# Kernel optimization log

Measured on AMD Instinct MI355X. Metric: run time of the kernel, lower is better.

## Reference

```python
import jax, jax.numpy as jnp
import numpy as np

N, R, D = 2048, 4, 256
TEMPERATURE = 1.0
CLAMP_MIN = 1e-8


def setup_inputs() -> dict:
    key = jax.random.key(0)
    a = jax.random.normal(key, (N, R, D), dtype=jnp.float32)
    return {"a": a}


def reference(a):
    n, r, d = a.shape
    # Full pairwise Gram tensor over (input i, context j) x (input k, context l)
    sim = jnp.einsum('ijd,kld->ikjl', a, a) / TEMPERATURE          # [N,N,r,r]
    # detached row-max over l for stability (matches sim.detach().max(-1, keepdim=True))
    sim_max = jax.lax.stop_gradient(jnp.max(sim, axis=-1, keepdims=True))
    dp = jnp.exp(sim - sim_max)                                    # [N,N,r,r]

    # Positive pairs: i == k, j != l
    diag = jnp.einsum('iijl->ijl', dp)                             # [N,r,r]
    offdiag_jl = ~jnp.eye(r, dtype=bool)                           # [r,r]
    sim_pos = jnp.sum(diag * offdiag_jl, axis=(1, 2)) / (r * (r - 1))  # [N]

    # Negative pairs: i != k, all (j,l); square then clamp, then per-i mean
    sq = jnp.maximum(jnp.square(dp), CLAMP_MIN)                    # [N,N,r,r]
    diag_sq = jnp.sum(jnp.maximum(jnp.square(diag), CLAMP_MIN), axis=(1, 2))  # [N]
    sim_neg = (jnp.sum(sq, axis=(1, 2, 3)) - diag_sq) / ((n - 1) * r * r)     # [N]

    lora_loss = -2.0 * sim_pos + sim_neg                           # [N]
    return jnp.mean(lora_loss)                                     # 'mean' reduction -> scalar
```

## Files before the change

### kernel.cpp

```cpp
#include <hip/hip_runtime.h>


#define PD   8192
#define KB   256
#define BM   128
#define BK   32
#define NIT  (KB / BK)

typedef __bf16 bf16x8 __attribute__((ext_vector_type(8)));
typedef float f32x4 __attribute__((ext_vector_type(4)));

__device__ __forceinline__ void gload16(const void* g, void* l) {
    __builtin_amdgcn_global_load_lds(
        (const __attribute__((address_space(1))) unsigned int*)g,
        (__attribute__((address_space(3))) unsigned int*)l, 16, 0, 0);
}

__device__ __forceinline__ int swz(int row) { return ((row >> 1) & 3) << 4; }

__device__ __forceinline__ float quadmax(float x) {
    int v = __builtin_amdgcn_mov_dpp(__builtin_bit_cast(int, x), 0xB1, 0xF, 0xF, true);
    float m = fmaxf(x, __builtin_bit_cast(float, v));
    v = __builtin_amdgcn_mov_dpp(__builtin_bit_cast(int, m), 0x4E, 0xF, 0xF, true);
    return fmaxf(m, __builtin_bit_cast(float, v));
}

__global__ __launch_bounds__(256)
void cvt_bf16(const float* __restrict__ A, __bf16* __restrict__ W,
              float* __restrict__ out) {
    const int idx = blockIdx.x * 256 + threadIdx.x;
    if (idx == 0) *out = 0.f;
    const float4 v0 = reinterpret_cast<const float4*>(A)[idx * 2];
    const float4 v1 = reinterpret_cast<const float4*>(A)[idx * 2 + 1];
    bf16x8 h;
    h[0] = (__bf16)v0.x; h[1] = (__bf16)v0.y; h[2] = (__bf16)v0.z; h[3] = (__bf16)v0.w;
    h[4] = (__bf16)v1.x; h[5] = (__bf16)v1.y; h[6] = (__bf16)v1.z; h[7] = (__bf16)v1.w;
    *reinterpret_cast<bf16x8*>(W + (size_t)idx * 8) = h;
}

__global__ __launch_bounds__(512)
void evd_mfma(const __bf16* __restrict__ W, float* __restrict__ out)
{
    __shared__ __bf16 lds[2][3][BM * BK];
    __shared__ float wsum[8];

    const int nid = (blockIdx.z * gridDim.y + blockIdx.y) * gridDim.x + blockIdx.x;
    const int id  = (nid & 7) * 132 + (nid >> 3);
    const int xx  = id % 33;
    const int yzq = id / 33;
    const int yy  = yzq & 15;
    const int zz  = yzq >> 4;
    int rp, px;
    if (xx < 32 - yy) { rp = yy;      px = xx; }
    else              { rp = 31 - yy; px = xx - (32 - yy); }
    const int bi  = 2 * rp + zz;
    const int bkL = bi + 2 * px;
    int bkR = bkL + 1;
    const bool validR = (bkR < 64);
    if (!validR) bkR = bkL;

    const int tid = threadIdx.x;
    const int lane = tid & 63, w = tid >> 6;
    const int g = w >> 2;
    const int sub = w & 3, wr = sub >> 1, wc = sub & 1;
    const int row0 = bi * BM;
    const int bk   = g ? bkR : bkL;
    const int col0 = bk * BM;
    const bool valid = g ? validR : true;

    const int ar = tid >> 2;
    const int ax = (tid & 3) * 16;
    const int gaA = (row0 + ar) * (KB * 2) + (ax ^ swz(ar));
    const int t2  = tid & 255;
    const int br0 = t2 >> 2, br1 = 64 + br0;
    const int bx  = (t2 & 3) * 16;
    const int colB = (w < 4 ? bkL : bkR) * BM;
    const int gaB0 = (colB + br0) * (KB * 2) + (bx ^ swz(br0));
    const int gaB1 = (colB + br1) * (KB * 2) + (bx ^ swz(br1));
    const char* gW = (const char*)W;
    const int dA = w * 1024;
    const int dB = 8192 + g * 8192 + (w & 3) * 1024;

    const int fr = lane & 15, kq = lane >> 4;
    int aOff[4], bOff[4];
#pragma unroll
    for (int m = 0; m < 4; ++m) {
        const int ra = wr * 64 + m * 16 + fr;
        const int rb = wc * 64 + m * 16 + fr;
        aOff[m] = ra * 64 + ((kq * 16) ^ swz(ra));
        bOff[m] = 8192 + g * 8192 + rb * 64 + ((kq * 16) ^ swz(rb));
    }

    f32x4 acc[4][4];
#pragma unroll
    for (int m = 0; m < 4; ++m)
#pragma unroll
        for (int n = 0; n < 4; ++n)
#pragma unroll
            for (int q = 0; q < 4; ++q) acc[m][n][q] = 0.f;

    auto stage = [&](int t, int b) {
        const int kb2 = t * (BK * 2);
        char* base = (char*)&lds[b][0][0];
        gload16(gW + gaA  + kb2, base + dA);
        gload16(gW + gaB0 + kb2, base + dB);
        gload16(gW + gaB1 + kb2, base + dB + 4096);
    };

    stage(0, 0);
    stage(1, 1);

#pragma unroll
    for (int t = 0; t < NIT; ++t) {
        if (t == NIT - 1) asm volatile("s_waitcnt vmcnt(0)" ::: "memory");
        else              asm volatile("s_waitcnt vmcnt(3)" ::: "memory");
        __builtin_amdgcn_s_barrier();

        const char* base = (const char*)&lds[t & 1][0][0];
        bf16x8 af[4], bfr[4];
#pragma unroll
        for (int m = 0; m < 4; ++m) {
            af[m]  = *(const bf16x8*)(base + aOff[m]);
            bfr[m] = *(const bf16x8*)(base + bOff[m]);
        }
        if (t + 2 < NIT) {
            asm volatile("s_waitcnt lgkmcnt(0)" ::: "memory");
            __builtin_amdgcn_s_barrier();
            stage(t + 2, t & 1);
        }
        __builtin_amdgcn_s_setprio(1);
#pragma unroll
        for (int m = 0; m < 4; ++m)
#pragma unroll
            for (int n = 0; n < 4; ++n)
                acc[m][n] = __builtin_amdgcn_mfma_f32_16x16x32_bf16(af[m], bfr[n], acc[m][n], 0, 0, 0);
        __builtin_amdgcn_s_setprio(0);
    }

    const float C_NEG = 1.0f / (2048.0f * 2047.0f * 16.0f);
    const float C_POS = 2.0f / (2048.0f * 12.0f);
    const float SCL = 2.0f * 1.4426950408889634f;
    const bool diag = (bi == bk);
    const bool ik = ((lane >> 4) == ((lane & 15) >> 2));
    float nsum = 0.f, psum = 0.f;

#pragma unroll
    for (int m = 0; m < 4; ++m) {
#pragma unroll
        for (int n = 0; n < 4; ++n) {
            float yv[4];
#pragma unroll
            for (int q = 0; q < 4; ++q) yv[q] = SCL * acc[m][n][q];
            const bool dfrag = diag && (wr == wc) && (m == n);
#pragma unroll
            for (int r = 0; r < 4; ++r) {
                const float d2 = yv[r] - quadmax(yv[r]);
                if (dfrag) {
                    const float dp = __builtin_amdgcn_exp2f(0.5f * d2);
                    if (ik) {
                        if (r != (lane & 3)) psum += dp;
                    } else {
                        nsum += fmaxf(dp * dp, 1e-8f);
                    }
                } else {
                    nsum += fmaxf(__builtin_amdgcn_exp2f(d2), 1e-8f);
                }
            }
            if (!diag) {
                const float ymax = fmaxf(fmaxf(fmaxf(yv[0], yv[1]), yv[2]), yv[3]);
#pragma unroll
                for (int r = 0; r < 4; ++r)
                    nsum += fmaxf(__builtin_amdgcn_exp2f(yv[r] - ymax), 1e-8f);
            }
        }
    }

    float contrib = valid ? (C_NEG * nsum - C_POS * psum) : 0.f;

#pragma unroll
    for (int off = 32; off; off >>= 1) contrib += __shfl_down(contrib, off);
    if (lane == 0) wsum[w] = contrib;
    __syncthreads();
    if (tid == 0) {
        float s = 0.f;
#pragma unroll
        for (int i = 0; i < 8; ++i) s += wsum[i];
        atomicAdd(out, s);
    }
}

extern "C" void kernel_launch(void* const* d_in, const int* in_sizes, int n_in,
                              void* d_out, int out_size, void* d_ws, size_t ws_size,
                              hipStream_t stream) {
    const float* A = (const float*)d_in[0];
    float* out = (float*)d_out;
    __bf16* W = (__bf16*)d_ws;
    cvt_bf16<<<(PD * KB / 8) / 256, 256, 0, stream>>>(A, W, out);
    dim3 grid(33, 16, 2);
    evd_mfma<<<grid, 512, 0, stream>>>(W, out);
}
```

Before: 92.82 us.

## Fuse fp32-to-bf16 conversion into Gram kernel with register-staged LDS loads

Removes the separate conversion kernel and bf16 workspace. The main kernel now loads fp32 rows into registers, converts them to bf16 and writes them into swizzled LDS, with a register-prefetch pipeline of depth one. The output is zeroed with a memset instead of inside the old kernel. This saves a launch and a workspace round trip, but it doubles global read bytes per tile (fp32), spends VGPRs on staging, and drops the async global-to-LDS double-stage prefetch.

```diff
diff --git a/kernel.cpp b/kernel.cpp
--- a/kernel.cpp
+++ b/kernel.cpp
@@ -2,21 +2,22 @@
 
 
 #define PD   8192
-#define KB   256
+#define DDIM 256
 #define BM   128
 #define BK   32
-#define NIT  (KB / BK)
+#define NIT  (DDIM / BK)
 
 typedef __bf16 bf16x8 __attribute__((ext_vector_type(8)));
 typedef float f32x4 __attribute__((ext_vector_type(4)));
 
-__device__ __forceinline__ void gload16(const void* g, void* l) {
-    __builtin_amdgcn_global_load_lds(
-        (const __attribute__((address_space(1))) unsigned int*)g,
-        (__attribute__((address_space(3))) unsigned int*)l, 16, 0, 0);
+__device__ __forceinline__ int swz(int row) { return ((row >> 1) & 3) << 4; }
+
+__device__ __forceinline__ bf16x8 pack8(float4 x, float4 y) {
+    bf16x8 h;
+    h[0] = (__bf16)x.x; h[1] = (__bf16)x.y; h[2] = (__bf16)x.z; h[3] = (__bf16)x.w;
+    h[4] = (__bf16)y.x; h[5] = (__bf16)y.y; h[6] = (__bf16)y.z; h[7] = (__bf16)y.w;
+    return h;
 }
-
-__device__ __forceinline__ int swz(int row) { return ((row >> 1) & 3) << 4; }
 
 __device__ __forceinline__ float quadmax(float x) {
     int v = __builtin_amdgcn_mov_dpp(__builtin_bit_cast(int, x), 0xB1, 0xF, 0xF, true);
@@ -25,21 +26,8 @@
     return fmaxf(m, __builtin_bit_cast(float, v));
 }
 
-__global__ __launch_bounds__(256)
-void cvt_bf16(const float* __restrict__ A, __bf16* __restrict__ W,
-              float* __restrict__ out) {
-    const int idx = blockIdx.x * 256 + threadIdx.x;
-    if (idx == 0) *out = 0.f;
-    const float4 v0 = reinterpret_cast<const float4*>(A)[idx * 2];
-    const float4 v1 = reinterpret_cast<const float4*>(A)[idx * 2 + 1];
-    bf16x8 h;
-    h[0] = (__bf16)v0.x; h[1] = (__bf16)v0.y; h[2] = (__bf16)v0.z; h[3] = (__bf16)v0.w;
-    h[4] = (__bf16)v1.x; h[5] = (__bf16)v1.y; h[6] = (__bf16)v1.z; h[7] = (__bf16)v1.w;
-    *reinterpret_cast<bf16x8*>(W + (size_t)idx * 8) = h;
-}
-
 __global__ __launch_bounds__(512)
-void evd_mfma(const __bf16* __restrict__ W, float* __restrict__ out)
+void evd_fused(const float* __restrict__ A, float* __restrict__ out)
 {
     __shared__ __bf16 lds[2][3][BM * BK];
     __shared__ float wsum[8];
@@ -65,21 +53,18 @@
     const int sub = w & 3, wr = sub >> 1, wc = sub & 1;
     const int row0 = bi * BM;
     const int bk   = g ? bkR : bkL;
-    const int col0 = bk * BM;
     const bool valid = g ? validR : true;
 
-    const int ar = tid >> 2;
-    const int ax = (tid & 3) * 16;
-    const int gaA = (row0 + ar) * (KB * 2) + (ax ^ swz(ar));
-    const int t2  = tid & 255;
-    const int br0 = t2 >> 2, br1 = 64 + br0;
-    const int bx  = (t2 & 3) * 16;
-    const int colB = (w < 4 ? bkL : bkR) * BM;
-    const int gaB0 = (colB + br0) * (KB * 2) + (bx ^ swz(br0));
-    const int gaB1 = (colB + br1) * (KB * 2) + (bx ^ swz(br1));
-    const char* gW = (const char*)W;
-    const int dA = w * 1024;
-    const int dB = 8192 + g * 8192 + (w & 3) * 1024;
+    const int arow = tid >> 2, aunit = tid & 3;
+    const float* gA = A + (size_t)(row0 + arow) * DDIM + aunit * 8;
+    const int wA = arow * 64 + ((aunit * 16) ^ swz(arow));
+    const int t2 = tid & 255, brow = t2 >> 1;
+    const int u0 = (t2 & 1) * 2, u1 = u0 + 1;
+    const int colB = (tid < 256 ? bkL : bkR) * BM;
+    const float* gB = A + (size_t)(colB + brow) * DDIM;
+    const int bSlab = 8192 + (tid >= 256) * 8192;
+    const int wB0 = bSlab + brow * 64 + ((u0 * 16) ^ swz(brow));
+    const int wB1 = bSlab + brow * 64 + ((u1 * 16) ^ swz(brow));
 
     const int fr = lane & 15, kq = lane >> 4;
     int aOff[4], bOff[4];
@@ -99,34 +84,36 @@
 #pragma unroll
             for (int q = 0; q < 4; ++q) acc[m][n][q] = 0.f;
 
-    auto stage = [&](int t, int b) {
-        const int kb2 = t * (BK * 2);
+    float4 ra0, ra1, rb0, rb1, rb2, rb3;
+    auto issue = [&](int t) {
+        const int kc = t * BK;
+        ra0 = *(const float4*)(gA + kc);
+        ra1 = *(const float4*)(gA + kc + 4);
+        rb0 = *(const float4*)(gB + kc + u0 * 8);
+        rb1 = *(const float4*)(gB + kc + u0 * 8 + 4);
+        rb2 = *(const float4*)(gB + kc + u1 * 8);
+        rb3 = *(const float4*)(gB + kc + u1 * 8 + 4);
+    };
+    auto cvtWrite = [&](int b) {
         char* base = (char*)&lds[b][0][0];
-        gload16(gW + gaA  + kb2, base + dA);
-        gload16(gW + gaB0 + kb2, base + dB);
-        gload16(gW + gaB1 + kb2, base + dB + 4096);
+        *(bf16x8*)(base + wA)  = pack8(ra0, ra1);
+        *(bf16x8*)(base + wB0) = pack8(rb0, rb1);
+        *(bf16x8*)(base + wB1) = pack8(rb2, rb3);
     };
 
-    stage(0, 0);
-    stage(1, 1);
+    issue(0);
+    cvtWrite(0);
+    __syncthreads();
 
 #pragma unroll
     for (int t = 0; t < NIT; ++t) {
-        if (t == NIT - 1) asm volatile("s_waitcnt vmcnt(0)" ::: "memory");
-        else              asm volatile("s_waitcnt vmcnt(3)" ::: "memory");
-        __builtin_amdgcn_s_barrier();
-
+        if (t + 1 < NIT) issue(t + 1);
         const char* base = (const char*)&lds[t & 1][0][0];
         bf16x8 af[4], bfr[4];
 #pragma unroll
         for (int m = 0; m < 4; ++m) {
             af[m]  = *(const bf16x8*)(base + aOff[m]);
             bfr[m] = *(const bf16x8*)(base + bOff[m]);
-        }
-        if (t + 2 < NIT) {
-            asm volatile("s_waitcnt lgkmcnt(0)" ::: "memory");
-            __builtin_amdgcn_s_barrier();
-            stage(t + 2, t & 1);
         }
         __builtin_amdgcn_s_setprio(1);
 #pragma unroll
@@ -135,6 +122,10 @@
             for (int n = 0; n < 4; ++n)
                 acc[m][n] = __builtin_amdgcn_mfma_f32_16x16x32_bf16(af[m], bfr[n], acc[m][n], 0, 0, 0);
         __builtin_amdgcn_s_setprio(0);
+        if (t + 1 < NIT) {
+            cvtWrite((t + 1) & 1);
+            __syncthreads();
+        }
     }
 
     const float C_NEG = 1.0f / (2048.0f * 2047.0f * 16.0f);
@@ -194,8 +185,7 @@
                               hipStream_t stream) {
     const float* A = (const float*)d_in[0];
     float* out = (float*)d_out;
-    __bf16* W = (__bf16*)d_ws;
-    cvt_bf16<<<(PD * KB / 8) / 256, 256, 0, stream>>>(A, W, out);
+    hipMemsetAsync(out, 0, sizeof(float), stream);
     dim3 grid(33, 16, 2);
-    evd_mfma<<<grid, 512, 0, stream>>>(W, out);
+    evd_fused<<<grid, 512, 0, stream>>>(A, out);
 }
```

After: 132.6 us. +42.8%, slower.
